# Kernel tuning notes

Measured on AMD Instinct MI355X. Metric: run time of the kernel, lower is better.

The kernel has to match this reference:

```python
import jax, jax.numpy as jnp
import numpy as np

SEQ_LEN, BATCH, TAG = 512, 1024, 64
START_IDX, END_IDX = 0, 1
NEG_INF = -10000.0


def setup_inputs() -> dict:
    key = jax.random.key(0)
    k1, k2, k3 = jax.random.split(key, 3)
    feats = jax.random.normal(k1, (SEQ_LEN, BATCH, TAG), dtype=jnp.float32)
    # variable-length sequences: valid prefix lengths in [SEQ_LEN//2, SEQ_LEN]
    lens = jax.random.randint(k2, (BATCH,), SEQ_LEN // 2, SEQ_LEN + 1)
    mask = (jnp.arange(SEQ_LEN)[:, None] < lens[None, :]).astype(jnp.float32)  # (S, B)
    # transition ~ xavier_normal_ then clamp START row / END column (reset_parameters)
    std = float(np.sqrt(2.0 / (TAG + TAG)))
    transition = jax.random.normal(k3, (TAG, TAG), dtype=jnp.float32) * std
    transition = transition.at[START_IDX, :].set(NEG_INF)
    transition = transition.at[:, END_IDX].set(NEG_INF)
    return {"feats": feats, "mask": mask, "transition": transition}


def reference(feats, mask, transition):
    # feats: (S, B, T), mask: (S, B), transition: (T, T) [next_tag, prev_tag]
    S, B, T = feats.shape
    alpha0 = jnp.full((B, T), NEG_INF, dtype=feats.dtype).at[:, START_IDX].set(0.0)

    def step(alpha, xs):
        feat, m = xs  # feat: (B, T), m: (B,)
        # alpha_score[b, next, prev] = alpha[b, prev] + transition[next, prev] + feat[b, next]
        score = alpha[:, None, :] + transition[None, :, :] + feat[:, :, None]
        new_alpha = jax.nn.logsumexp(score, axis=-1)  # (B, T)
        m = m[:, None]
        alpha = new_alpha * m + alpha * (1.0 - m)
        return alpha, None

    alpha, _ = jax.lax.scan(step, alpha0, (feats, mask))
    alpha = alpha + transition[END_IDX][None, :]
    return jax.nn.logsumexp(alpha, axis=-1)  # (B,)
```

## Files before the change

### kernel.cpp

```cpp
#include <hip/hip_runtime.h>

namespace {
constexpr int S_LEN = 512;
constexpr int BATCH = 1024;
constexpr int TAG = 64;
constexpr int START_IDX = 0;
constexpr int END_IDX = 1;
constexpr float NEG_INF = -10000.0f;
constexpr int CHUNK = 64;
constexpr float LN2F = 0.69314718055994530942f;

typedef float v2f __attribute__((ext_vector_type(2)));
typedef float v4f __attribute__((ext_vector_type(4)));

typedef const __attribute__((address_space(1))) void* gas_ptr;
typedef __attribute__((address_space(3))) void* las_ptr;

__device__ inline void gld_lds16(const float* g, float* l) {
  __builtin_amdgcn_global_load_lds((gas_ptr)(const void*)g, (las_ptr)(void*)l, 16, 0, 0);
}
}

__global__ __launch_bounds__(64, 1) void crf_fwd_kernel(
    const float* __restrict__ feats,
    const float* __restrict__ mask,
    const float* __restrict__ trans,
    float* __restrict__ out) {
  const int b = blockIdx.x;
  const int lane = threadIdx.x;

  __shared__ __align__(16) float fchunk[2][CHUNK * TAG];

  int L;
  {
    float sum = 0.0f;
#pragma unroll
    for (int k = 0; k < S_LEN / 64; ++k) sum += mask[(size_t)(lane + 64 * k) * BATCH + b];
#pragma unroll
    for (int off = 32; off >= 1; off >>= 1) sum += __shfl_xor(sum, off, 64);
    L = (int)(sum + 0.5f);
  }

  float Ee[TAG];
  {
    const float* row = trans + lane * TAG;
#pragma unroll
    for (int k = 0; k < TAG / 4; ++k) {
      v4f tv;
      __builtin_memcpy(&tv, row + 4 * k, sizeof(v4f));
      Ee[4 * k + 0] = __expf(tv.x);
      Ee[4 * k + 1] = __expf(tv.y);
      Ee[4 * k + 2] = __expf(tv.z);
      Ee[4 * k + 3] = __expf(tv.w);
    }
  }

  const float* gstage0 =
      feats + ((size_t)(lane >> 4) * BATCH + b) * TAG + ((lane & 15) << 2);

  auto stage_chunk = [&](int base_s, int nb) {
    const float* g0 = gstage0 + (size_t)base_s * (BATCH * TAG);
#pragma unroll
    for (int q = 0; q < 16; ++q) {
      gld_lds16(g0 + (size_t)(4 * q) * (BATCH * TAG), &fchunk[nb][q * 256]);
    }
  };

  float p = (lane == START_IDX) ? 1.0f : 0.0f;
  int etot = 0;

  stage_chunk(0, 0);
  asm volatile("s_waitcnt vmcnt(0)" ::: "memory");
  __builtin_amdgcn_sched_barrier(0);
  __builtin_amdgcn_wave_barrier();

  auto step = [&](float ex) {
    const unsigned pu = __float_as_uint(p);

    const unsigned pb = __builtin_amdgcn_readlane(pu, 2);
    const unsigned eb = (pb == 0u) ? 127u : (pb >> 23);
    etot += (int)eb - 127;
    const float scale = __uint_as_float((254u - eb) << 23);
    const float cg = ex * scale;

    float a0 = 0.f, a1 = 0.f, a2 = 0.f, a3 = 0.f;
    float a4 = 0.f, a5 = 0.f, a6 = 0.f, a7 = 0.f;
#pragma unroll
    for (int k = 0; k < TAG; k += 8) {
      a0 = __builtin_fmaf(__uint_as_float(__builtin_amdgcn_readlane(pu, k + 0)), Ee[k + 0], a0);
      a1 = __builtin_fmaf(__uint_as_float(__builtin_amdgcn_readlane(pu, k + 1)), Ee[k + 1], a1);
      a2 = __builtin_fmaf(__uint_as_float(__builtin_amdgcn_readlane(pu, k + 2)), Ee[k + 2], a2);
      a3 = __builtin_fmaf(__uint_as_float(__builtin_amdgcn_readlane(pu, k + 3)), Ee[k + 3], a3);
      a4 = __builtin_fmaf(__uint_as_float(__builtin_amdgcn_readlane(pu, k + 4)), Ee[k + 4], a4);
      a5 = __builtin_fmaf(__uint_as_float(__builtin_amdgcn_readlane(pu, k + 5)), Ee[k + 5], a5);
      a6 = __builtin_fmaf(__uint_as_float(__builtin_amdgcn_readlane(pu, k + 6)), Ee[k + 6], a6);
      a7 = __builtin_fmaf(__uint_as_float(__builtin_amdgcn_readlane(pu, k + 7)), Ee[k + 7], a7);
    }
    const float t = ((a0 + a1) + (a2 + a3)) + ((a4 + a5) + (a6 + a7));
    p = t * cg;
  };

  for (int c = 0;; ++c) {
    const int base = c * CHUNK;
    int n = L - base;
    if (n <= 0) break;
    if (n > CHUNK) n = CHUNK;

    const int nbase = base + CHUNK;
    if (nbase < S_LEN) stage_chunk(nbase, (c + 1) & 1);

    const float* fb = &fchunk[c & 1][0];

    auto group8 = [&](int s0) {
      float ex[8];
#pragma unroll
      for (int i = 0; i < 8; ++i) ex[i] = fb[(s0 + i) * TAG + lane];
#pragma unroll
      for (int i = 0; i < 8; ++i) ex[i] = __expf(ex[i]);
#pragma unroll
      for (int i = 0; i < 8; ++i) step(ex[i]);
    };

    if (n == CHUNK) {
      for (int g = 0; g < CHUNK / 8; ++g) group8(8 * g);
    } else {
      const int full = n >> 3;
      for (int g = 0; g < full; ++g) group8(8 * g);
      for (int i = full * 8; i < n; ++i) {
        step(__expf(fb[i * TAG + lane]));
      }
      break;
    }

    if (nbase >= L) break;

    asm volatile("s_waitcnt vmcnt(0)" ::: "memory");
    __builtin_amdgcn_sched_barrier(0);
    __builtin_amdgcn_wave_barrier();
  }

  asm volatile("s_waitcnt vmcnt(0)" ::: "memory");

  {
    const float a = (float)etot * LN2F + __logf(p) + trans[END_IDX * TAG + lane];
    float mx = a;
#pragma unroll
    for (int off = 32; off >= 1; off >>= 1) mx = fmaxf(mx, __shfl_xor(mx, off, 64));
    float e = __expf(a - mx);
#pragma unroll
    for (int off = 32; off >= 1; off >>= 1) e += __shfl_xor(e, off, 64);
    if (lane == 0) out[b] = mx + __logf(e);
  }
}

extern "C" void kernel_launch(void* const* d_in, const int* in_sizes, int n_in,
                              void* d_out, int out_size, void* d_ws, size_t ws_size,
                              hipStream_t stream) {
  const float* feats = (const float*)d_in[0];
  const float* mask = (const float*)d_in[1];
  const float* trans = (const float*)d_in[2];
  float* out = (float*)d_out;
  crf_fwd_kernel<<<dim3(BATCH), dim3(64), 0, stream>>>(feats, mask, trans, out);
}
```

Measured before the change: 271.6 us.

## Split matvec broadcast between LDS vector reads and readlane for half the tags

Each step now writes the scaled probability vector to LDS and reads the first 32 entries back as broadcast v4f loads feeding packed v2f FMAs. The remaining 32 entries still use scalar readlane broadcasts. The aim is to overlap LDS latency with the SALU readlane path and to use packed FP32 math, shortening the serial per-step critical path. It adds an LDS round trip and wave barriers every step, and that latency sits on the recurrence's dependency chain.

```diff
diff --git a/kernel.cpp b/kernel.cpp
--- a/kernel.cpp
+++ b/kernel.cpp
@@ -30,6 +30,7 @@
   const int lane = threadIdx.x;
 
   __shared__ __align__(16) float fchunk[2][CHUNK * TAG];
+  __shared__ __align__(16) float p_lds[TAG];
 
   int L;
   {
@@ -41,17 +42,25 @@
     L = (int)(sum + 0.5f);
   }
 
-  float Ee[TAG];
+  v2f El[16];
+  float Eu[32];
   {
     const float* row = trans + lane * TAG;
 #pragma unroll
-    for (int k = 0; k < TAG / 4; ++k) {
+    for (int k = 0; k < 8; ++k) {
       v4f tv;
       __builtin_memcpy(&tv, row + 4 * k, sizeof(v4f));
-      Ee[4 * k + 0] = __expf(tv.x);
-      Ee[4 * k + 1] = __expf(tv.y);
-      Ee[4 * k + 2] = __expf(tv.z);
-      Ee[4 * k + 3] = __expf(tv.w);
+      El[2 * k]     = v2f{__expf(tv.x), __expf(tv.y)};
+      El[2 * k + 1] = v2f{__expf(tv.z), __expf(tv.w)};
+    }
+#pragma unroll
+    for (int k = 0; k < 8; ++k) {
+      v4f tv;
+      __builtin_memcpy(&tv, row + 32 + 4 * k, sizeof(v4f));
+      Eu[4 * k + 0] = __expf(tv.x);
+      Eu[4 * k + 1] = __expf(tv.y);
+      Eu[4 * k + 2] = __expf(tv.z);
+      Eu[4 * k + 3] = __expf(tv.w);
     }
   }
 
@@ -83,21 +92,62 @@
     const float scale = __uint_as_float((254u - eb) << 23);
     const float cg = ex * scale;
 
-    float a0 = 0.f, a1 = 0.f, a2 = 0.f, a3 = 0.f;
-    float a4 = 0.f, a5 = 0.f, a6 = 0.f, a7 = 0.f;
-#pragma unroll
-    for (int k = 0; k < TAG; k += 8) {
-      a0 = __builtin_fmaf(__uint_as_float(__builtin_amdgcn_readlane(pu, k + 0)), Ee[k + 0], a0);
-      a1 = __builtin_fmaf(__uint_as_float(__builtin_amdgcn_readlane(pu, k + 1)), Ee[k + 1], a1);
-      a2 = __builtin_fmaf(__uint_as_float(__builtin_amdgcn_readlane(pu, k + 2)), Ee[k + 2], a2);
-      a3 = __builtin_fmaf(__uint_as_float(__builtin_amdgcn_readlane(pu, k + 3)), Ee[k + 3], a3);
-      a4 = __builtin_fmaf(__uint_as_float(__builtin_amdgcn_readlane(pu, k + 4)), Ee[k + 4], a4);
-      a5 = __builtin_fmaf(__uint_as_float(__builtin_amdgcn_readlane(pu, k + 5)), Ee[k + 5], a5);
-      a6 = __builtin_fmaf(__uint_as_float(__builtin_amdgcn_readlane(pu, k + 6)), Ee[k + 6], a6);
-      a7 = __builtin_fmaf(__uint_as_float(__builtin_amdgcn_readlane(pu, k + 7)), Ee[k + 7], a7);
-    }
-    const float t = ((a0 + a1) + (a2 + a3)) + ((a4 + a5) + (a6 + a7));
-    p = t * cg;
+    p_lds[lane] = p;
+    __builtin_amdgcn_wave_barrier();
+    v4f q0, q1, q2, q3, q4, q5, q6, q7;
+    __builtin_memcpy(&q0, p_lds + 0,  sizeof(v4f));
+    __builtin_memcpy(&q1, p_lds + 4,  sizeof(v4f));
+    __builtin_memcpy(&q2, p_lds + 8,  sizeof(v4f));
+    __builtin_memcpy(&q3, p_lds + 12, sizeof(v4f));
+    __builtin_memcpy(&q4, p_lds + 16, sizeof(v4f));
+    __builtin_memcpy(&q5, p_lds + 20, sizeof(v4f));
+    __builtin_memcpy(&q6, p_lds + 24, sizeof(v4f));
+    __builtin_memcpy(&q7, p_lds + 28, sizeof(v4f));
+
+    float t0 = 0.f, t1 = 0.f, t2 = 0.f, t3 = 0.f;
+    {
+      float r[16];
+#pragma unroll
+      for (int k = 0; k < 16; ++k)
+        r[k] = __uint_as_float(__builtin_amdgcn_readlane(pu, 32 + k));
+#pragma unroll
+      for (int k = 0; k < 16; k += 4) {
+        t0 = __builtin_fmaf(r[k + 0], Eu[k + 0], t0);
+        t1 = __builtin_fmaf(r[k + 1], Eu[k + 1], t1);
+        t2 = __builtin_fmaf(r[k + 2], Eu[k + 2], t2);
+        t3 = __builtin_fmaf(r[k + 3], Eu[k + 3], t3);
+      }
+    }
+    {
+      float r[16];
+#pragma unroll
+      for (int k = 0; k < 16; ++k)
+        r[k] = __uint_as_float(__builtin_amdgcn_readlane(pu, 48 + k));
+#pragma unroll
+      for (int k = 0; k < 16; k += 4) {
+        t0 = __builtin_fmaf(r[k + 0], Eu[16 + k + 0], t0);
+        t1 = __builtin_fmaf(r[k + 1], Eu[16 + k + 1], t1);
+        t2 = __builtin_fmaf(r[k + 2], Eu[16 + k + 2], t2);
+        t3 = __builtin_fmaf(r[k + 3], Eu[16 + k + 3], t3);
+      }
+    }
+
+    v2f c0 = {0.f, 0.f}, c1 = {0.f, 0.f}, c2 = {0.f, 0.f}, c3 = {0.f, 0.f};
+    c0 += v2f{q0.x, q0.y} * El[0];  c1 += v2f{q0.z, q0.w} * El[1];
+    c2 += v2f{q1.x, q1.y} * El[2];  c3 += v2f{q1.z, q1.w} * El[3];
+    c0 += v2f{q2.x, q2.y} * El[4];  c1 += v2f{q2.z, q2.w} * El[5];
+    c2 += v2f{q3.x, q3.y} * El[6];  c3 += v2f{q3.z, q3.w} * El[7];
+    c0 += v2f{q4.x, q4.y} * El[8];  c1 += v2f{q4.z, q4.w} * El[9];
+    c2 += v2f{q5.x, q5.y} * El[10]; c3 += v2f{q5.z, q5.w} * El[11];
+    c0 += v2f{q6.x, q6.y} * El[12]; c1 += v2f{q6.z, q6.w} * El[13];
+    c2 += v2f{q7.x, q7.y} * El[14]; c3 += v2f{q7.z, q7.w} * El[15];
+
+    const v2f cs = (c0 + c1) + (c2 + c3);
+    const float tl = cs.x + cs.y;
+    const float tu = (t0 + t1) + (t2 + t3);
+    p = (tl + tu) * cg;
+
+    __builtin_amdgcn_wave_barrier();
   };
 
   for (int c = 0;; ++c) {
```

Result: no change. 274.7 us (+1.1%).

## Broadcast alpha via LDS with packed FMA and renormalize every fourth step

Applied to the files above, without the earlier changes.

Each step now writes the probability vector to a double-buffered LDS slot and every lane reads it back with vector LDS loads, replacing the 64 per-step readlane broadcasts. The matvec uses packed two-wide float FMAs over v2f pairs of the exponentiated transition row. Exponent renormalization now runs once per group of four steps instead of every step. This trades the serialized SALU readlane chain for LDS store/load latency on the critical dependency chain, and skipping renormalization on three of four steps risks overflow or underflow in p.

```diff
diff --git a/kernel.cpp b/kernel.cpp
--- a/kernel.cpp
+++ b/kernel.cpp
@@ -30,6 +30,7 @@
   const int lane = threadIdx.x;
 
   __shared__ __align__(16) float fchunk[2][CHUNK * TAG];
+  __shared__ __align__(16) float p_lds[2][TAG];
 
   int L;
   {
@@ -41,17 +42,15 @@
     L = (int)(sum + 0.5f);
   }
 
-  float Ee[TAG];
+  v2f El[TAG / 2];
   {
     const float* row = trans + lane * TAG;
 #pragma unroll
     for (int k = 0; k < TAG / 4; ++k) {
       v4f tv;
       __builtin_memcpy(&tv, row + 4 * k, sizeof(v4f));
-      Ee[4 * k + 0] = __expf(tv.x);
-      Ee[4 * k + 1] = __expf(tv.y);
-      Ee[4 * k + 2] = __expf(tv.z);
-      Ee[4 * k + 3] = __expf(tv.w);
+      El[2 * k]     = v2f{__expf(tv.x), __expf(tv.y)};
+      El[2 * k + 1] = v2f{__expf(tv.z), __expf(tv.w)};
     }
   }
 
@@ -74,30 +73,55 @@
   __builtin_amdgcn_sched_barrier(0);
   __builtin_amdgcn_wave_barrier();
 
-  auto step = [&](float ex) {
+  auto do_step = [&](float cgi, int par, bool renorm) {
     const unsigned pu = __float_as_uint(p);
+    p_lds[par][lane] = p;
+    __builtin_amdgcn_wave_barrier();
 
-    const unsigned pb = __builtin_amdgcn_readlane(pu, 2);
-    const unsigned eb = (pb == 0u) ? 127u : (pb >> 23);
-    etot += (int)eb - 127;
-    const float scale = __uint_as_float((254u - eb) << 23);
-    const float cg = ex * scale;
+    float cgl = cgi;
+    if (renorm) {
+      const unsigned pb = __builtin_amdgcn_readlane(pu, 2);
+      const unsigned eb = (pb == 0u) ? 127u : (pb >> 23);
+      etot += (int)eb - 127;
+      cgl = cgi * __uint_as_float((254u - eb) << 23);
+    }
 
-    float a0 = 0.f, a1 = 0.f, a2 = 0.f, a3 = 0.f;
-    float a4 = 0.f, a5 = 0.f, a6 = 0.f, a7 = 0.f;
+    const float* pl = &p_lds[par][0];
+    v2f a0 = {0.f, 0.f}, a1 = {0.f, 0.f}, a2 = {0.f, 0.f}, a3 = {0.f, 0.f};
+    v2f a4 = {0.f, 0.f}, a5 = {0.f, 0.f}, a6 = {0.f, 0.f}, a7 = {0.f, 0.f};
 #pragma unroll
-    for (int k = 0; k < TAG; k += 8) {
-      a0 = __builtin_fmaf(__uint_as_float(__builtin_amdgcn_readlane(pu, k + 0)), Ee[k + 0], a0);
-      a1 = __builtin_fmaf(__uint_as_float(__builtin_amdgcn_readlane(pu, k + 1)), Ee[k + 1], a1);
-      a2 = __builtin_fmaf(__uint_as_float(__builtin_amdgcn_readlane(pu, k + 2)), Ee[k + 2], a2);
-      a3 = __builtin_fmaf(__uint_as_float(__builtin_amdgcn_readlane(pu, k + 3)), Ee[k + 3], a3);
-      a4 = __builtin_fmaf(__uint_as_float(__builtin_amdgcn_readlane(pu, k + 4)), Ee[k + 4], a4);
-      a5 = __builtin_fmaf(__uint_as_float(__builtin_amdgcn_readlane(pu, k + 5)), Ee[k + 5], a5);
-      a6 = __builtin_fmaf(__uint_as_float(__builtin_amdgcn_readlane(pu, k + 6)), Ee[k + 6], a6);
-      a7 = __builtin_fmaf(__uint_as_float(__builtin_amdgcn_readlane(pu, k + 7)), Ee[k + 7], a7);
+    for (int k = 0; k < 4; ++k) {
+      v4f q0, q1, q2, q3;
+      __builtin_memcpy(&q0, pl + 16 * k + 0,  sizeof(v4f));
+      __builtin_memcpy(&q1, pl + 16 * k + 4,  sizeof(v4f));
+      __builtin_memcpy(&q2, pl + 16 * k + 8,  sizeof(v4f));
+      __builtin_memcpy(&q3, pl + 16 * k + 12, sizeof(v4f));
+      a0 += v2f{q0.x, q0.y} * El[8 * k + 0];
+      a1 += v2f{q0.z, q0.w} * El[8 * k + 1];
+      a2 += v2f{q1.x, q1.y} * El[8 * k + 2];
+      a3 += v2f{q1.z, q1.w} * El[8 * k + 3];
+      a4 += v2f{q2.x, q2.y} * El[8 * k + 4];
+      a5 += v2f{q2.z, q2.w} * El[8 * k + 5];
+      a6 += v2f{q3.x, q3.y} * El[8 * k + 6];
+      a7 += v2f{q3.z, q3.w} * El[8 * k + 7];
     }
-    const float t = ((a0 + a1) + (a2 + a3)) + ((a4 + a5) + (a6 + a7));
-    p = t * cg;
+    const v2f s0 = (a0 + a1) + (a2 + a3);
+    const v2f s1 = (a4 + a5) + (a6 + a7);
+    const v2f st = s0 + s1;
+    const float t = st.x + st.y;
+    p = t * cgl;
+  };
+
+  auto group4 = [&](const float* fb, int s0) {
+    float cg[4];
+#pragma unroll
+    for (int i = 0; i < 4; ++i) cg[i] = fb[(s0 + i) * TAG + lane];
+#pragma unroll
+    for (int i = 0; i < 4; ++i) cg[i] = __expf(cg[i]);
+    do_step(cg[0], 0, true);
+    do_step(cg[1], 1, false);
+    do_step(cg[2], 0, false);
+    do_step(cg[3], 1, false);
   };
 
   for (int c = 0;; ++c) {
@@ -111,23 +135,13 @@
 
     const float* fb = &fchunk[c & 1][0];
 
-    auto group8 = [&](int s0) {
-      float ex[8];
-#pragma unroll
-      for (int i = 0; i < 8; ++i) ex[i] = fb[(s0 + i) * TAG + lane];
-#pragma unroll
-      for (int i = 0; i < 8; ++i) ex[i] = __expf(ex[i]);
-#pragma unroll
-      for (int i = 0; i < 8; ++i) step(ex[i]);
-    };
-
     if (n == CHUNK) {
-      for (int g = 0; g < CHUNK / 8; ++g) group8(8 * g);
+      for (int g = 0; g < CHUNK / 4; ++g) group4(fb, 4 * g);
     } else {
-      const int full = n >> 3;
-      for (int g = 0; g < full; ++g) group8(8 * g);
-      for (int i = full * 8; i < n; ++i) {
-        step(__expf(fb[i * TAG + lane]));
+      const int full = n >> 2;
+      for (int g = 0; g < full; ++g) group4(fb, 4 * g);
+      for (int i = full * 4; i < n; ++i) {
+        do_step(__expf(fb[i * TAG + lane]), i & 1, true);
       }
       break;
     }
```

After: 282.4 us. 4.0% more time.

## Replace per-step readlane broadcast with DPP/swizzle butterfly all-gather

Applied to the files above, without the earlier changes.

Each recurrence step now gathers all 64 lanes' alpha values with one ds_bpermute, ds_swizzle and a cascade of DPP moves, instead of 64 scalar readlane operations. The transition exponentials are pre-permuted per lane to match the lane-dependent gather order. The goal is to cut the serialized SALU readlane traffic and the VALU-to-SGPR dependency stalls on the critical path. In exchange it adds LDS-path latency from bpermute and swizzle, plus 64 extra VGPRs for the gathered values.

```diff
diff --git a/kernel.cpp b/kernel.cpp
--- a/kernel.cpp
+++ b/kernel.cpp
@@ -10,7 +10,6 @@
 constexpr int CHUNK = 64;
 constexpr float LN2F = 0.69314718055994530942f;
 
-typedef float v2f __attribute__((ext_vector_type(2)));
 typedef float v4f __attribute__((ext_vector_type(4)));
 
 typedef const __attribute__((address_space(1))) void* gas_ptr;
@@ -18,6 +17,30 @@
 
 __device__ inline void gld_lds16(const float* g, float* l) {
   __builtin_amdgcn_global_load_lds((gas_ptr)(const void*)g, (las_ptr)(void*)l, 16, 0, 0);
+}
+
+template <int CTRL>
+__device__ __forceinline__ unsigned dppmov(unsigned v) {
+  return (unsigned)__builtin_amdgcn_mov_dpp((int)v, CTRL, 0xF, 0xF, false);
+}
+
+__device__ __forceinline__ unsigned swz_x16(unsigned v) {
+  return (unsigned)__builtin_amdgcn_ds_swizzle((int)v, 0x401F);
+}
+
+__device__ __forceinline__ void allgather64(unsigned x, int lane, unsigned u[64]) {
+  u[0]  = x;
+  u[32] = (unsigned)__builtin_amdgcn_ds_bpermute((lane ^ 32) << 2, (int)x);
+  u[16] = swz_x16(u[0]);
+  u[48] = swz_x16(u[32]);
+#pragma unroll
+  for (int h = 0; h < 64; h += 16) u[h + 8] = dppmov<0x128>(u[h]);
+#pragma unroll
+  for (int h = 0; h < 64; h += 8)  u[h + 4] = dppmov<0x124>(u[h]);
+#pragma unroll
+  for (int h = 0; h < 64; h += 4)  u[h + 2] = dppmov<0x4E>(u[h]);
+#pragma unroll
+  for (int h = 0; h < 64; h += 2)  u[h + 1] = dppmov<0xB1>(u[h]);
 }
 }
 
@@ -41,18 +64,13 @@
     L = (int)(sum + 0.5f);
   }
 
-  float Ee[TAG];
+  float Eg[64];
   {
-    const float* row = trans + lane * TAG;
+    unsigned gi[64];
+    allgather64((unsigned)lane, lane, gi);
+    const float* trow = trans + lane * TAG;
 #pragma unroll
-    for (int k = 0; k < TAG / 4; ++k) {
-      v4f tv;
-      __builtin_memcpy(&tv, row + 4 * k, sizeof(v4f));
-      Ee[4 * k + 0] = __expf(tv.x);
-      Ee[4 * k + 1] = __expf(tv.y);
-      Ee[4 * k + 2] = __expf(tv.z);
-      Ee[4 * k + 3] = __expf(tv.w);
-    }
+    for (int r = 0; r < 64; ++r) Eg[r] = __expf(trow[gi[r]]);
   }
 
   const float* gstage0 =
@@ -77,24 +95,26 @@
   auto step = [&](float ex) {
     const unsigned pu = __float_as_uint(p);
 
+    unsigned u[64];
+    allgather64(pu, lane, u);
+
     const unsigned pb = __builtin_amdgcn_readlane(pu, 2);
     const unsigned eb = (pb == 0u) ? 127u : (pb >> 23);
     etot += (int)eb - 127;
-    const float scale = __uint_as_float((254u - eb) << 23);
-    const float cg = ex * scale;
+    const float cg = ex * __uint_as_float((254u - eb) << 23);
 
     float a0 = 0.f, a1 = 0.f, a2 = 0.f, a3 = 0.f;
     float a4 = 0.f, a5 = 0.f, a6 = 0.f, a7 = 0.f;
 #pragma unroll
-    for (int k = 0; k < TAG; k += 8) {
-      a0 = __builtin_fmaf(__uint_as_float(__builtin_amdgcn_readlane(pu, k + 0)), Ee[k + 0], a0);
-      a1 = __builtin_fmaf(__uint_as_float(__builtin_amdgcn_readlane(pu, k + 1)), Ee[k + 1], a1);
-      a2 = __builtin_fmaf(__uint_as_float(__builtin_amdgcn_readlane(pu, k + 2)), Ee[k + 2], a2);
-      a3 = __builtin_fmaf(__uint_as_float(__builtin_amdgcn_readlane(pu, k + 3)), Ee[k + 3], a3);
-      a4 = __builtin_fmaf(__uint_as_float(__builtin_amdgcn_readlane(pu, k + 4)), Ee[k + 4], a4);
-      a5 = __builtin_fmaf(__uint_as_float(__builtin_amdgcn_readlane(pu, k + 5)), Ee[k + 5], a5);
-      a6 = __builtin_fmaf(__uint_as_float(__builtin_amdgcn_readlane(pu, k + 6)), Ee[k + 6], a6);
-      a7 = __builtin_fmaf(__uint_as_float(__builtin_amdgcn_readlane(pu, k + 7)), Ee[k + 7], a7);
+    for (int r = 0; r < 64; r += 8) {
+      a0 = __builtin_fmaf(__uint_as_float(u[r + 0]), Eg[r + 0], a0);
+      a1 = __builtin_fmaf(__uint_as_float(u[r + 1]), Eg[r + 1], a1);
+      a2 = __builtin_fmaf(__uint_as_float(u[r + 2]), Eg[r + 2], a2);
+      a3 = __builtin_fmaf(__uint_as_float(u[r + 3]), Eg[r + 3], a3);
+      a4 = __builtin_fmaf(__uint_as_float(u[r + 4]), Eg[r + 4], a4);
+      a5 = __builtin_fmaf(__uint_as_float(u[r + 5]), Eg[r + 5], a5);
+      a6 = __builtin_fmaf(__uint_as_float(u[r + 6]), Eg[r + 6], a6);
+      a7 = __builtin_fmaf(__uint_as_float(u[r + 7]), Eg[r + 7], a7);
     }
     const float t = ((a0 + a1) + (a2 + a3)) + ((a4 + a5) + (a6 + a7));
     p = t * cg;
```

Result: slower. 283.1 us (+4.2%).
